# Performance work log

Hardware: AMD Instinct MI355X
Metric: run time of the kernel (lower is better)

## Reference

```python
import jax, jax.numpy as jnp
import numpy as np

N, E, SEQ, IN, HID, OUT = 2048, 65536, 5, 32, 64, 16
EPS = 1e-5


def setup_inputs() -> dict:
    ks = jax.random.split(jax.random.key(0), 16)
    def w(k, shape):
        return jax.random.normal(k, shape, jnp.float32) / np.float32(np.sqrt(shape[0]))
    z = lambda n: jnp.zeros((n,), jnp.float32)
    return dict(
        x=jax.random.normal(ks[0], (SEQ, N, IN), jnp.float32),
        edge_weight=jax.random.uniform(ks[1], (E,), jnp.float32),
        Wcz=w(ks[2], (IN, HID)), bcz=z(HID), Wlz=w(ks[3], (2 * HID, HID)), blz=z(HID),
        Wcr=w(ks[4], (IN, HID)), bcr=z(HID), Wlr=w(ks[5], (2 * HID, HID)), blr=z(HID),
        Wch=w(ks[6], (IN, HID)), bch=z(HID), Wlh=w(ks[7], (2 * HID, HID)), blh=z(HID),
        Wred=w(ks[8], (SEQ * HID, HID)), bred=z(HID),
        Wc1=w(ks[9], (HID, HID)), bc1=z(HID), Wc2=w(ks[10], (HID, HID)), bc2=z(HID),
        g1=jnp.ones((HID,), jnp.float32), be1=z(HID),
        g2=jnp.ones((HID,), jnp.float32), be2=z(HID),
        Wout=w(ks[11], (HID, OUT)), bout=z(OUT),
        Wi1=w(ks[12], (2 * HID, HID)), bi1=z(HID),
        Wi2=w(ks[13], (HID, 1)), bi2=z(1),
        edge_index=jax.random.randint(ks[14], (2, E), 0, N),
    )


def _layer_norm(h, g, b):
    mu = jnp.mean(h, -1, keepdims=True)
    var = jnp.mean((h - mu) ** 2, -1, keepdims=True)
    return (h - mu) * jax.lax.rsqrt(var + EPS) * g + b


def _forward(x, edge_weight, Wcz, bcz, Wlz, blz, Wcr, bcr, Wlr, blr,
             Wch, bch, Wlh, blh, Wred, bred, Wc1, bc1, Wc2, bc2,
             g1, be1, g2, be2, Wout, bout, Wi1, bi1, Wi2, bi2, edge_index):
    src, dst = edge_index[0], edge_index[1]
    # GCN symmetric normalization with self-loops (weight 1.0); shared by all convs.
    deg = jax.ops.segment_sum(edge_weight, dst, num_segments=N) + 1.0
    dinv = jax.lax.rsqrt(deg)
    norm = dinv[src] * edge_weight * dinv[dst]  # [E]
    dself = dinv * dinv                          # [N] self-loop coefficient

    def gcn(h, W, b):
        hw = h @ W
        agg = jax.ops.segment_sum(norm[:, None] * hw[src], dst, num_segments=N)
        return agg + dself[:, None] * hw + b

    # TGCN per timestep. The original passes no hidden state, so H resets to 0
    # each call: H_t = (1 - Z) * tanh(candidate); reset gate R is multiplied by
    # H=0 and has no effect (its params get zero gradient, matching torch).
    hs = []
    for t in range(SEQ):  # SEQ=5, fixed small loop
        Zg = jax.nn.sigmoid(gcn(x[t], Wcz, bcz) @ Wlz[:HID] + blz)
        Ht = jnp.tanh(gcn(x[t], Wch, bch) @ Wlh[:HID] + blh)
        hs.append((1.0 - Zg) * Ht)
    h = jnp.stack(hs, axis=1).reshape(N, SEQ * HID)
    h = h @ Wred + bred
    emb = h  # intermediate embeddings for the interaction predictor
    h = gcn(h, Wc1, bc1)
    h = jax.nn.relu(_layer_norm(h, g1, be1))  # dropout = identity in eval
    h = gcn(h, Wc2, bc2)
    h = jax.nn.relu(_layer_norm(h, g2, be2))
    node_pred = h @ Wout + bout
    # InteractionPredictor: cat([e_i, e_j]) @ Wi1 == e_i @ Wi1[:H] + e_j @ Wi1[H:]
    a = emb @ Wi1[:HID]
    bj = emb @ Wi1[HID:]
    hp = jax.nn.relu(a[:, None, :] + bj[None, :, :] + bi1)  # [N, N, HID]
    scores = (hp @ Wi2)[..., 0] + bi2[0]                     # [N, N]
    return node_pred, scores


def reference(x, edge_index, edge_weight, Wcz, bcz, Wlz, blz, Wcr, bcr, Wlr, blr,
              Wch, bch, Wlh, blh, Wred, bred, Wc1, bc1, Wc2, bc2,
              g1, be1, g2, be2, Wout, bout, Wi1, bi1, Wi2, bi2):
    return _forward(x, edge_weight, Wcz, bcz, Wlz, blz, Wcr, bcr, Wlr, blr,
                    Wch, bch, Wlh, blh, Wred, bred, Wc1, bc1, Wc2, bc2,
                    g1, be1, g2, be2, Wout, bout, Wi1, bi1, Wi2, bi2, edge_index)
```

## Files before the change

### kernel.cpp

```cpp
#include <hip/hip_runtime.h>
#include <math.h>

#define N_NODES 2048
#define N_EDGES 65536
#define SEQL 5
#define IN_F 32
#define HID 64
#define OUT_F 16
#define LN_EPS 1e-5f
#define CAP 128

__global__ __launch_bounds__(256) void k_build(
        const int* __restrict__ ei, const float* __restrict__ ew,
        const float* __restrict__ Wcz, const float* __restrict__ Wlz,
        const float* __restrict__ bcz, const float* __restrict__ blz,
        const float* __restrict__ Wch, const float* __restrict__ Wlh,
        const float* __restrict__ bch, const float* __restrict__ blh,
        int* __restrict__ cnt, float2* __restrict__ cedge,
        float* __restrict__ Wzp, float* __restrict__ Whp, float* __restrict__ bUV){
    int b = blockIdx.x, t = threadIdx.x;
    if (b < 256){
        int e = b * 256 + t;
        int s = ei[e], d = ei[N_EDGES + e];
        int pos = atomicAdd(&cnt[d], 1);
        if (pos < CAP){
            float2 v;
            v.x = __int_as_float(s);
            v.y = ew[e];
            cedge[(d << 7) + pos] = v;
        }
    } else {
        const float* Wc = (b == 256) ? Wcz : Wch;
        const float* Wl = (b == 256) ? Wlz : Wlh;
        const float* bc = (b == 256) ? bcz : bch;
        const float* bl = (b == 256) ? blz : blh;
        float* Wp = (b == 256) ? Wzp : Whp;
        for (int idx = t; idx < IN_F*HID; idx += 256){
            int i = idx >> 6, f = idx & 63;
            float s = 0.f;
            #pragma unroll 8
            for (int k = 0; k < HID; ++k) s += Wc[i*HID+k] * Wl[k*HID+f];
            Wp[idx] = s;
        }
        if (t < HID){
            float s = bl[t];
            for (int k = 0; k < HID; ++k) s += bc[k] * Wl[k*HID+t];
            bUV[(b-256)*HID + t] = s;
        }
    }
}

__global__ void k_dinv(const int* __restrict__ cnt, const float2* __restrict__ cedge,
                       float* __restrict__ dinv, float* __restrict__ dself){
    int n = blockIdx.x * 64 + threadIdx.x;
    int m = min(cnt[n], CAP);
    float s = 1.f;
    for (int i = 0; i < m; ++i) s += cedge[(n << 7) + i].y;
    float iv = 1.f / sqrtf(s);
    dinv[n] = iv;
    dself[n] = iv * iv;
}

__global__ __launch_bounds__(320) void k_gate(const float* __restrict__ x,
        const float* __restrict__ dinv, const float* __restrict__ dself,
        const int* __restrict__ cnt, const float2* __restrict__ cedge,
        const float* __restrict__ bUV, const float* __restrict__ Wzp, const float* __restrict__ Whp,
        const float* __restrict__ Wred, const float* __restrict__ bred,
        const float* __restrict__ Wi1, const float* __restrict__ bi1, const float* __restrict__ Wc1,
        float* __restrict__ ag, float* __restrict__ bjp, float* __restrict__ hw1y){
    int n = blockIdx.x;
    int tid = threadIdx.x;
    __shared__ float part[40*SEQL*IN_F];
    __shared__ float axs[SEQL][IN_F];
    __shared__ float hs[SEQL][HID];
    __shared__ float pw[SEQL][HID];
    __shared__ float hemb[HID];
    const int slot = tid >> 3, fl = tid & 7;
    const int f = tid & 63, t = tid >> 6;
    int m = min(cnt[n], CAP);
    float dvn = dinv[n], dsn = dself[n];
    const float4* X4 = (const float4*)x;
    float4 a0 = {0,0,0,0}, a1 = {0,0,0,0}, a2 = {0,0,0,0}, a3 = {0,0,0,0}, a4 = {0,0,0,0};
    for (int p = slot; p < m; p += 40){
        float2 ed = cedge[(n << 7) + p];
        int s = __float_as_int(ed.x);
        float c = ed.y * dinv[s];
        float4 x0 = X4[(0*N_NODES + s)*8 + fl];
        float4 x1 = X4[(1*N_NODES + s)*8 + fl];
        float4 x2 = X4[(2*N_NODES + s)*8 + fl];
        float4 x3 = X4[(3*N_NODES + s)*8 + fl];
        float4 x4v= X4[(4*N_NODES + s)*8 + fl];
        a0.x += c*x0.x; a0.y += c*x0.y; a0.z += c*x0.z; a0.w += c*x0.w;
        a1.x += c*x1.x; a1.y += c*x1.y; a1.z += c*x1.z; a1.w += c*x1.w;
        a2.x += c*x2.x; a2.y += c*x2.y; a2.z += c*x2.z; a2.w += c*x2.w;
        a3.x += c*x3.x; a3.y += c*x3.y; a3.z += c*x3.z; a3.w += c*x3.w;
        a4.x += c*x4v.x; a4.y += c*x4v.y; a4.z += c*x4v.z; a4.w += c*x4v.w;
    }
    *(float4*)&part[(slot*SEQL + 0)*IN_F + fl*4] = a0;
    *(float4*)&part[(slot*SEQL + 1)*IN_F + fl*4] = a1;
    *(float4*)&part[(slot*SEQL + 2)*IN_F + fl*4] = a2;
    *(float4*)&part[(slot*SEQL + 3)*IN_F + fl*4] = a3;
    *(float4*)&part[(slot*SEQL + 4)*IN_F + fl*4] = a4;
    __syncthreads();
    if (tid < SEQL*IN_F){
        int tt = tid >> 5, ff = tid & 31;
        float ps = 0.f;
        #pragma unroll 8
        for (int sl = 0; sl < 40; ++sl) ps += part[(sl*SEQL + tt)*IN_F + ff];
        axs[tt][ff] = dsn * x[(tt*N_NODES + n)*IN_F + ff] + dvn * ps;
    }
    __syncthreads();
    {
        float zz = bUV[f], hh = bUV[HID + f];
        #pragma unroll
        for (int i = 0; i < IN_F; ++i){
            float a = axs[t][i];
            zz += a * Wzp[i*HID + f];
            hh += a * Whp[i*HID + f];
        }
        float z = 1.f / (1.f + expf(-zz));
        hs[t][f] = (1.f - z) * tanhf(hh);
    }
    __syncthreads();
    {   float pp = 0.f;
        #pragma unroll
        for (int k = 0; k < HID; ++k) pp += hs[t][k] * Wred[(t*HID + k)*HID + f];
        pw[t][f] = pp;
    }
    __syncthreads();
    if (tid < HID){
        float hr = bred[tid];
        #pragma unroll
        for (int t2 = 0; t2 < SEQL; ++t2) hr += pw[t2][tid];
        hemb[tid] = hr;
    }
    __syncthreads();
    if (t < 3){
        const float* W = (t == 0) ? Wi1 : (t == 1) ? (Wi1 + HID*HID) : Wc1;
        float acc = (t == 1) ? bi1[f] : 0.f;
        #pragma unroll
        for (int k = 0; k < HID; ++k) acc += hemb[k] * W[k*HID + f];
        if (t == 2) acc *= dvn;
        float* O = (t == 0) ? ag : (t == 1) ? bjp : hw1y;
        O[n*HID + f] = acc;
    }
}

__global__ __launch_bounds__(512) void k_gcn1s(
        const float* __restrict__ hw1y, const float* __restrict__ dinv,
        const int* __restrict__ cnt, const float2* __restrict__ cedge,
        const float* __restrict__ bc1, const float* __restrict__ g1, const float* __restrict__ be1,
        const float* __restrict__ Wc2, float* __restrict__ hw2y,
        const float* __restrict__ ag, const float* __restrict__ bjp,
        const float* __restrict__ Wi2, const float* __restrict__ bi2,
        float* __restrict__ outs){
    int blk = blockIdx.x;
    int tid = threadIdx.x;
    __shared__ float part[32*HID];
    __shared__ float hsh[HID];
    __shared__ float red8[8*HID];
    __shared__ float bs[64*65];
    __shared__ float wv[64];
    if (blk < N_NODES){
        int n = blk;
        const int slot = tid >> 4, fl = tid & 15;
        const int f = tid & 63, w = tid >> 6;
        int m = min(cnt[n], CAP);
        float dv = dinv[n];
        const float4* H4 = (const float4*)hw1y;
        float4 acc = {0,0,0,0};
        for (int p = slot; p < m; p += 32){
            float2 ed = cedge[(n << 7) + p];
            int s = __float_as_int(ed.x); float c = ed.y;
            float4 h = H4[s*16 + fl];
            acc.x += c*h.x; acc.y += c*h.y; acc.z += c*h.z; acc.w += c*h.w;
        }
        *(float4*)&part[slot*HID + fl*4] = acc;
        __syncthreads();
        if (w == 0){
            float g = hw1y[n*HID + f];
            #pragma unroll 8
            for (int sl = 0; sl < 32; ++sl) g += part[sl*HID + f];
            g = bc1[f] + dv * g;
            float sum = g;
            for (int o = 32; o > 0; o >>= 1) sum += __shfl_xor(sum, o, 64);
            float mu = sum * (1.f/64.f);
            float d = g - mu;
            float vs = d * d;
            for (int o = 32; o > 0; o >>= 1) vs += __shfl_xor(vs, o, 64);
            float var = vs * (1.f/64.f);
            float h = d * (1.f / sqrtf(var + LN_EPS)) * g1[f] + be1[f];
            hsh[f] = fmaxf(h, 0.f);
        }
        __syncthreads();
        float s = 0.f;
        #pragma unroll
        for (int k = 0; k < 8; ++k) s += hsh[w*8 + k] * Wc2[(w*8 + k)*HID + f];
        red8[w*HID + f] = s;
        __syncthreads();
        if (w == 0){
            float o = 0.f;
            #pragma unroll
            for (int k = 0; k < 8; ++k) o += red8[k*HID + f];
            hw2y[n*HID + f] = dv * o;
        }
    } else {
        int tl = blk - N_NODES;
        int j0 = (tl & 31) * 64;
        int i0 = (tl >> 5) * 32;
        for (int idx = tid; idx < 4096; idx += 512){
            int jj = idx >> 6, f = idx & 63;
            bs[jj*65 + f] = bjp[(j0 + jj)*HID + f];
        }
        if (tid < 64) wv[tid] = Wi2[tid];
        __syncthreads();
        int tj = tid & 63;
        int w = __builtin_amdgcn_readfirstlane(tid >> 6);
        const float* ar = ag + (i0 + w*4)*HID;
        float bi2v = bi2[0];
        float acc0 = 0.f, acc1 = 0.f, acc2 = 0.f, acc3 = 0.f;
        #pragma unroll
        for (int f = 0; f < 64; ++f){
            float bv = bs[tj*65 + f];
            float wf = wv[f];
            acc0 += fmaxf(ar[       f] + bv, 0.f) * wf;
            acc1 += fmaxf(ar[ 64 +  f] + bv, 0.f) * wf;
            acc2 += fmaxf(ar[128 +  f] + bv, 0.f) * wf;
            acc3 += fmaxf(ar[192 +  f] + bv, 0.f) * wf;
        }
        long ro = (long)(i0 + w*4) * N_NODES + j0 + tj;
        outs[ro                ] = acc0 + bi2v;
        outs[ro +     N_NODES  ] = acc1 + bi2v;
        outs[ro + 2L* N_NODES  ] = acc2 + bi2v;
        outs[ro + 3L* N_NODES  ] = acc3 + bi2v;
    }
}

__global__ __launch_bounds__(512) void k_gcn2s(
        const float* __restrict__ hw2y, const float* __restrict__ dinv,
        const int* __restrict__ cnt, const float2* __restrict__ cedge,
        const float* __restrict__ bc2, const float* __restrict__ g2, const float* __restrict__ be2,
        const float* __restrict__ Wout, const float* __restrict__ bout,
        const float* __restrict__ ag, const float* __restrict__ bjp,
        const float* __restrict__ Wi2, const float* __restrict__ bi2,
        float* __restrict__ outp, float* __restrict__ outs){
    int blk = blockIdx.x;
    int tid = threadIdx.x;
    __shared__ float part[32*HID];
    __shared__ float hsh[HID];
    __shared__ float bs[64*65];
    __shared__ float wv[64];
    if (blk < N_NODES){
        int n = blk;
        const int slot = tid >> 4, fl = tid & 15;
        const int f = tid & 63, w = tid >> 6;
        int m = min(cnt[n], CAP);
        float dv = dinv[n];
        const float4* H4 = (const float4*)hw2y;
        float4 acc = {0,0,0,0};
        for (int p = slot; p < m; p += 32){
            float2 ed = cedge[(n << 7) + p];
            int s = __float_as_int(ed.x); float c = ed.y;
            float4 h = H4[s*16 + fl];
            acc.x += c*h.x; acc.y += c*h.y; acc.z += c*h.z; acc.w += c*h.w;
        }
        *(float4*)&part[slot*HID + fl*4] = acc;
        __syncthreads();
        if (w == 0){
            float g = hw2y[n*HID + f];
            #pragma unroll 8
            for (int sl = 0; sl < 32; ++sl) g += part[sl*HID + f];
            g = bc2[f] + dv * g;
            float sum = g;
            for (int o = 32; o > 0; o >>= 1) sum += __shfl_xor(sum, o, 64);
            float mu = sum * (1.f/64.f);
            float d = g - mu;
            float vs = d * d;
            for (int o = 32; o > 0; o >>= 1) vs += __shfl_xor(vs, o, 64);
            float var = vs * (1.f/64.f);
            float h = d * (1.f / sqrtf(var + LN_EPS)) * g2[f] + be2[f];
            hsh[f] = fmaxf(h, 0.f);
        }
        __syncthreads();
        if (w == 0 && f < OUT_F){
            float s = bout[f];
            #pragma unroll
            for (int k = 0; k < HID; ++k) s += hsh[k] * Wout[k*OUT_F + f];
            outp[n*OUT_F + f] = s;
        }
    } else {
        int tl = blk - N_NODES + 1024;
        int j0 = (tl & 31) * 64;
        int i0 = (tl >> 5) * 32;
        for (int idx = tid; idx < 4096; idx += 512){
            int jj = idx >> 6, f = idx & 63;
            bs[jj*65 + f] = bjp[(j0 + jj)*HID + f];
        }
        if (tid < 64) wv[tid] = Wi2[tid];
        __syncthreads();
        int tj = tid & 63;
        int w = __builtin_amdgcn_readfirstlane(tid >> 6);
        const float* ar = ag + (i0 + w*4)*HID;
        float bi2v = bi2[0];
        float acc0 = 0.f, acc1 = 0.f, acc2 = 0.f, acc3 = 0.f;
        #pragma unroll
        for (int f = 0; f < 64; ++f){
            float bv = bs[tj*65 + f];
            float wf = wv[f];
            acc0 += fmaxf(ar[       f] + bv, 0.f) * wf;
            acc1 += fmaxf(ar[ 64 +  f] + bv, 0.f) * wf;
            acc2 += fmaxf(ar[128 +  f] + bv, 0.f) * wf;
            acc3 += fmaxf(ar[192 +  f] + bv, 0.f) * wf;
        }
        long ro = (long)(i0 + w*4) * N_NODES + j0 + tj;
        outs[ro                ] = acc0 + bi2v;
        outs[ro +     N_NODES  ] = acc1 + bi2v;
        outs[ro + 2L* N_NODES  ] = acc2 + bi2v;
        outs[ro + 3L* N_NODES  ] = acc3 + bi2v;
    }
}

extern "C" void kernel_launch(void* const* d_in, const int* in_sizes, int n_in,
                              void* d_out, int out_size, void* d_ws, size_t ws_size,
                              hipStream_t stream){
    const float* x   = (const float*)d_in[0];
    const float* ew  = (const float*)d_in[1];
    const float* Wcz = (const float*)d_in[2];  const float* bcz = (const float*)d_in[3];
    const float* Wlz = (const float*)d_in[4];  const float* blz = (const float*)d_in[5];
    const float* Wch = (const float*)d_in[10]; const float* bch = (const float*)d_in[11];
    const float* Wlh = (const float*)d_in[12]; const float* blh = (const float*)d_in[13];
    const float* Wred= (const float*)d_in[14]; const float* bred= (const float*)d_in[15];
    const float* Wc1 = (const float*)d_in[16]; const float* bc1 = (const float*)d_in[17];
    const float* Wc2 = (const float*)d_in[18]; const float* bc2 = (const float*)d_in[19];
    const float* g1  = (const float*)d_in[20]; const float* be1 = (const float*)d_in[21];
    const float* g2  = (const float*)d_in[22]; const float* be2 = (const float*)d_in[23];
    const float* Wout= (const float*)d_in[24]; const float* bout= (const float*)d_in[25];
    const float* Wi1 = (const float*)d_in[26]; const float* bi1 = (const float*)d_in[27];
    const float* Wi2 = (const float*)d_in[28]; const float* bi2 = (const float*)d_in[29];
    const int*  ei  = (const int*)d_in[30];

    float* w = (float*)d_ws;
    int*   cnt   = (int*)w;
    float* dinv  = w + 2048;
    float* dself = w + 4096;
    float2* cedge= (float2*)(w + 6144);
    float* Wzp   = w + 530432;
    float* Whp   = w + 532480;
    float* bUV   = w + 534528;
    float* ag    = w + 534656;
    float* bjp   = w + 665728;
    float* hw1y  = w + 796800;
    float* hw2y  = w + 927872;

    hipMemsetAsync(cnt, 0, 8192, stream);
    k_build<<<258, 256, 0, stream>>>(ei, ew, Wcz, Wlz, bcz, blz, Wch, Wlh, bch, blh,
                                     cnt, cedge, Wzp, Whp, bUV);
    k_dinv<<<32, 64, 0, stream>>>(cnt, cedge, dinv, dself);
    k_gate<<<N_NODES, 320, 0, stream>>>(x, dinv, dself, cnt, cedge, bUV, Wzp, Whp,
                                        Wred, bred, Wi1, bi1, Wc1, ag, bjp, hw1y);
    k_gcn1s<<<N_NODES + 1024, 512, 0, stream>>>(hw1y, dinv, cnt, cedge, bc1, g1, be1,
                                                Wc2, hw2y, ag, bjp, Wi2, bi2,
                                                (float*)d_out + N_NODES*OUT_F);
    k_gcn2s<<<N_NODES + 1024, 512, 0, stream>>>(hw2y, dinv, cnt, cedge, bc2, g2, be2,
                                                Wout, bout, ag, bjp, Wi2, bi2,
                                                (float*)d_out, (float*)d_out + N_NODES*OUT_F);
}
```

Before: 211.7 us.

## Process one node per wavefront in GCN layers using shuffle reductions

The GCN aggregation, layer norm and following matmul now map one node to each 64-lane wavefront (8 nodes per block) instead of one node per 512-thread block. All reductions and the small matmuls go through cross-lane shuffles instead of shared memory and __syncthreads. The node-block count drops from 2048 to 256 per kernel, and shared memory is only declared in the score-tile branch. This aims to remove idle threads and barrier overhead in the node phase, at the cost of fewer parallel lanes per node during edge gathering.

```diff
diff --git a/kernel.cpp b/kernel.cpp
--- a/kernel.cpp
+++ b/kernel.cpp
@@ -156,56 +156,62 @@
         float* __restrict__ outs){
     int blk = blockIdx.x;
     int tid = threadIdx.x;
-    __shared__ float part[32*HID];
-    __shared__ float hsh[HID];
-    __shared__ float red8[8*HID];
-    __shared__ float bs[64*65];
-    __shared__ float wv[64];
-    if (blk < N_NODES){
-        int n = blk;
-        const int slot = tid >> 4, fl = tid & 15;
-        const int f = tid & 63, w = tid >> 6;
+    if (blk < 256){
+        int w = tid >> 6, l = tid & 63;
+        int n = (blk << 3) + w;
+        int slot = l >> 4, fl = l & 15;
         int m = min(cnt[n], CAP);
         float dv = dinv[n];
         const float4* H4 = (const float4*)hw1y;
-        float4 acc = {0,0,0,0};
-        for (int p = slot; p < m; p += 32){
+        float4 acc = {0.f,0.f,0.f,0.f};
+        if (slot == 0) acc = H4[n*16 + fl];
+        for (int p = slot; p < m; p += 4){
             float2 ed = cedge[(n << 7) + p];
             int s = __float_as_int(ed.x); float c = ed.y;
             float4 h = H4[s*16 + fl];
             acc.x += c*h.x; acc.y += c*h.y; acc.z += c*h.z; acc.w += c*h.w;
         }
-        *(float4*)&part[slot*HID + fl*4] = acc;
-        __syncthreads();
-        if (w == 0){
-            float g = hw1y[n*HID + f];
-            #pragma unroll 8
-            for (int sl = 0; sl < 32; ++sl) g += part[sl*HID + f];
-            g = bc1[f] + dv * g;
-            float sum = g;
-            for (int o = 32; o > 0; o >>= 1) sum += __shfl_xor(sum, o, 64);
-            float mu = sum * (1.f/64.f);
-            float d = g - mu;
-            float vs = d * d;
-            for (int o = 32; o > 0; o >>= 1) vs += __shfl_xor(vs, o, 64);
-            float var = vs * (1.f/64.f);
-            float h = d * (1.f / sqrtf(var + LN_EPS)) * g1[f] + be1[f];
-            hsh[f] = fmaxf(h, 0.f);
-        }
-        __syncthreads();
-        float s = 0.f;
-        #pragma unroll
-        for (int k = 0; k < 8; ++k) s += hsh[w*8 + k] * Wc2[(w*8 + k)*HID + f];
-        red8[w*HID + f] = s;
-        __syncthreads();
-        if (w == 0){
-            float o = 0.f;
-            #pragma unroll
-            for (int k = 0; k < 8; ++k) o += red8[k*HID + f];
-            hw2y[n*HID + f] = dv * o;
-        }
+        acc.x += __shfl_xor(acc.x, 16); acc.y += __shfl_xor(acc.y, 16);
+        acc.z += __shfl_xor(acc.z, 16); acc.w += __shfl_xor(acc.w, 16);
+        acc.x += __shfl_xor(acc.x, 32); acc.y += __shfl_xor(acc.y, 32);
+        acc.z += __shfl_xor(acc.z, 32); acc.w += __shfl_xor(acc.w, 32);
+        float4 b4 = ((const float4*)bc1)[fl];
+        float4 g;
+        g.x = b4.x + dv*acc.x; g.y = b4.y + dv*acc.y;
+        g.z = b4.z + dv*acc.z; g.w = b4.w + dv*acc.w;
+        float s4 = g.x + g.y + g.z + g.w;
+        s4 += __shfl_xor(s4, 1); s4 += __shfl_xor(s4, 2);
+        s4 += __shfl_xor(s4, 4); s4 += __shfl_xor(s4, 8);
+        float mu = s4 * (1.f/64.f);
+        float4 d;
+        d.x = g.x - mu; d.y = g.y - mu; d.z = g.z - mu; d.w = g.w - mu;
+        float v4 = d.x*d.x + d.y*d.y + d.z*d.z + d.w*d.w;
+        v4 += __shfl_xor(v4, 1); v4 += __shfl_xor(v4, 2);
+        v4 += __shfl_xor(v4, 4); v4 += __shfl_xor(v4, 8);
+        float rs = 1.f / sqrtf(v4 * (1.f/64.f) + LN_EPS);
+        float4 gm = ((const float4*)g1)[fl], be = ((const float4*)be1)[fl];
+        float4 h4;
+        h4.x = fmaxf(d.x*rs*gm.x + be.x, 0.f);
+        h4.y = fmaxf(d.y*rs*gm.y + be.y, 0.f);
+        h4.z = fmaxf(d.z*rs*gm.z + be.z, 0.f);
+        h4.w = fmaxf(d.w*rs*gm.w + be.w, 0.f);
+        float o = 0.f;
+        #pragma unroll 4
+        for (int gk = 0; gk < 16; ++gk){
+            float hb0 = __shfl(h4.x, gk);
+            float hb1 = __shfl(h4.y, gk);
+            float hb2 = __shfl(h4.z, gk);
+            float hb3 = __shfl(h4.w, gk);
+            o += hb0 * Wc2[(4*gk+0)*HID + l];
+            o += hb1 * Wc2[(4*gk+1)*HID + l];
+            o += hb2 * Wc2[(4*gk+2)*HID + l];
+            o += hb3 * Wc2[(4*gk+3)*HID + l];
+        }
+        hw2y[n*HID + l] = dv * o;
     } else {
-        int tl = blk - N_NODES;
+        __shared__ float bs[64*65];
+        __shared__ float wv[64];
+        int tl = blk - 256;
         int j0 = (tl & 31) * 64;
         int i0 = (tl >> 5) * 32;
         for (int idx = tid; idx < 4096; idx += 512){
@@ -246,50 +252,63 @@
         float* __restrict__ outp, float* __restrict__ outs){
     int blk = blockIdx.x;
     int tid = threadIdx.x;
-    __shared__ float part[32*HID];
-    __shared__ float hsh[HID];
-    __shared__ float bs[64*65];
-    __shared__ float wv[64];
-    if (blk < N_NODES){
-        int n = blk;
-        const int slot = tid >> 4, fl = tid & 15;
-        const int f = tid & 63, w = tid >> 6;
+    if (blk < 256){
+        int w = tid >> 6, l = tid & 63;
+        int n = (blk << 3) + w;
+        int slot = l >> 4, fl = l & 15;
         int m = min(cnt[n], CAP);
         float dv = dinv[n];
         const float4* H4 = (const float4*)hw2y;
-        float4 acc = {0,0,0,0};
-        for (int p = slot; p < m; p += 32){
+        float4 acc = {0.f,0.f,0.f,0.f};
+        if (slot == 0) acc = H4[n*16 + fl];
+        for (int p = slot; p < m; p += 4){
             float2 ed = cedge[(n << 7) + p];
             int s = __float_as_int(ed.x); float c = ed.y;
             float4 h = H4[s*16 + fl];
             acc.x += c*h.x; acc.y += c*h.y; acc.z += c*h.z; acc.w += c*h.w;
         }
-        *(float4*)&part[slot*HID + fl*4] = acc;
-        __syncthreads();
-        if (w == 0){
-            float g = hw2y[n*HID + f];
-            #pragma unroll 8
-            for (int sl = 0; sl < 32; ++sl) g += part[sl*HID + f];
-            g = bc2[f] + dv * g;
-            float sum = g;
-            for (int o = 32; o > 0; o >>= 1) sum += __shfl_xor(sum, o, 64);
-            float mu = sum * (1.f/64.f);
-            float d = g - mu;
-            float vs = d * d;
-            for (int o = 32; o > 0; o >>= 1) vs += __shfl_xor(vs, o, 64);
-            float var = vs * (1.f/64.f);
-            float h = d * (1.f / sqrtf(var + LN_EPS)) * g2[f] + be2[f];
-            hsh[f] = fmaxf(h, 0.f);
-        }
-        __syncthreads();
-        if (w == 0 && f < OUT_F){
-            float s = bout[f];
-            #pragma unroll
-            for (int k = 0; k < HID; ++k) s += hsh[k] * Wout[k*OUT_F + f];
-            outp[n*OUT_F + f] = s;
-        }
+        acc.x += __shfl_xor(acc.x, 16); acc.y += __shfl_xor(acc.y, 16);
+        acc.z += __shfl_xor(acc.z, 16); acc.w += __shfl_xor(acc.w, 16);
+        acc.x += __shfl_xor(acc.x, 32); acc.y += __shfl_xor(acc.y, 32);
+        acc.z += __shfl_xor(acc.z, 32); acc.w += __shfl_xor(acc.w, 32);
+        float4 b4 = ((const float4*)bc2)[fl];
+        float4 g;
+        g.x = b4.x + dv*acc.x; g.y = b4.y + dv*acc.y;
+        g.z = b4.z + dv*acc.z; g.w = b4.w + dv*acc.w;
+        float s4 = g.x + g.y + g.z + g.w;
+        s4 += __shfl_xor(s4, 1); s4 += __shfl_xor(s4, 2);
+        s4 += __shfl_xor(s4, 4); s4 += __shfl_xor(s4, 8);
+        float mu = s4 * (1.f/64.f);
+        float4 d;
+        d.x = g.x - mu; d.y = g.y - mu; d.z = g.z - mu; d.w = g.w - mu;
+        float v4 = d.x*d.x + d.y*d.y + d.z*d.z + d.w*d.w;
+        v4 += __shfl_xor(v4, 1); v4 += __shfl_xor(v4, 2);
+        v4 += __shfl_xor(v4, 4); v4 += __shfl_xor(v4, 8);
+        float rs = 1.f / sqrtf(v4 * (1.f/64.f) + LN_EPS);
+        float4 gm = ((const float4*)g2)[fl], be = ((const float4*)be2)[fl];
+        float4 h4;
+        h4.x = fmaxf(d.x*rs*gm.x + be.x, 0.f);
+        h4.y = fmaxf(d.y*rs*gm.y + be.y, 0.f);
+        h4.z = fmaxf(d.z*rs*gm.z + be.z, 0.f);
+        h4.w = fmaxf(d.w*rs*gm.w + be.w, 0.f);
+        int f2 = l & 15;
+        float o = bout[f2];
+        #pragma unroll 4
+        for (int gk = 0; gk < 16; ++gk){
+            float hb0 = __shfl(h4.x, gk);
+            float hb1 = __shfl(h4.y, gk);
+            float hb2 = __shfl(h4.z, gk);
+            float hb3 = __shfl(h4.w, gk);
+            o += hb0 * Wout[(4*gk+0)*OUT_F + f2];
+            o += hb1 * Wout[(4*gk+1)*OUT_F + f2];
+            o += hb2 * Wout[(4*gk+2)*OUT_F + f2];
+            o += hb3 * Wout[(4*gk+3)*OUT_F + f2];
+        }
+        if (slot == 0) outp[n*OUT_F + f2] = o;
     } else {
-        int tl = blk - N_NODES + 1024;
+        __shared__ float bs[64*65];
+        __shared__ float wv[64];
+        int tl = blk - 256 + 1024;
         int j0 = (tl & 31) * 64;
         int i0 = (tl >> 5) * 32;
         for (int idx = tid; idx < 4096; idx += 512){
@@ -358,10 +377,10 @@
     k_dinv<<<32, 64, 0, stream>>>(cnt, cedge, dinv, dself);
     k_gate<<<N_NODES, 320, 0, stream>>>(x, dinv, dself, cnt, cedge, bUV, Wzp, Whp,
                                         Wred, bred, Wi1, bi1, Wc1, ag, bjp, hw1y);
-    k_gcn1s<<<N_NODES + 1024, 512, 0, stream>>>(hw1y, dinv, cnt, cedge, bc1, g1, be1,
-                                                Wc2, hw2y, ag, bjp, Wi2, bi2,
-                                                (float*)d_out + N_NODES*OUT_F);
-    k_gcn2s<<<N_NODES + 1024, 512, 0, stream>>>(hw2y, dinv, cnt, cedge, bc2, g2, be2,
-                                                Wout, bout, ag, bjp, Wi2, bi2,
-                                                (float*)d_out, (float*)d_out + N_NODES*OUT_F);
-}
+    k_gcn1s<<<256 + 1024, 512, 0, stream>>>(hw1y, dinv, cnt, cedge, bc1, g1, be1,
+                                            Wc2, hw2y, ag, bjp, Wi2, bi2,
+                                            (float*)d_out + N_NODES*OUT_F);
+    k_gcn2s<<<256 + 1024, 512, 0, stream>>>(hw2y, dinv, cnt, cedge, bc2, g2, be2,
+                                            Wout, bout, ag, bjp, Wi2, bi2,
+                                            (float*)d_out, (float*)d_out + N_NODES*OUT_F);
+}
```

Result: faster. 203.9 us (-3.7%).
